# Optimization experiments

Measured on AMD Instinct MI355X. Metric: run time of the kernel, lower is better.

Reference implementation:

```python
import jax, jax.numpy as jnp
import numpy as np


def _igd(x, pf):
    # pf: [M, d] reference front, x: [N, d] candidate set
    # squared Euclidean distances via ||a||^2 + ||b||^2 - 2 a.b (cdist expansion)
    pf_sq = jnp.sum(pf * pf, axis=1, keepdims=True)          # [M, 1]
    x_sq = jnp.sum(x * x, axis=1, keepdims=True).T            # [1, N]
    cross = pf @ x.T                                          # [M, N]
    d2 = jnp.maximum(pf_sq + x_sq - 2.0 * cross, 0.0)
    dist = jnp.sqrt(d2)                                       # [M, N]
    # IGD: mean over reference points of min distance to candidate set
    return jnp.mean(jnp.min(dist, axis=1))


def setup_inputs() -> dict:
    key = jax.random.key(0)
    k1, k2 = jax.random.split(key)
    N, M, D = 16384, 16384, 64
    x = jax.random.normal(k1, (N, D), dtype=jnp.float32)
    pf = jax.random.normal(k2, (M, D), dtype=jnp.float32)
    return {"x": x, "pf": pf}


def reference(x, pf):
    return _igd(x, pf)
```

## Files before the change

kernel.cpp:

```cpp
#include <hip/hip_runtime.h>


typedef float f32x16 __attribute__((ext_vector_type(16)));
typedef int i32x8 __attribute__((ext_vector_type(8)));
typedef unsigned long long u64;

#define DIM 64
#define NSPLIT 12
#define UNITB 2048
#define CHUNKU 8
#define CHUNKB (CHUNKU * UNITB)
#define MTILE 256

union BFrag { u64 q[4]; i32x8 v; };

__device__ inline unsigned char enc_e4m3(float f) {
    unsigned int u = __float_as_uint(f);
    unsigned int s = (u >> 24) & 0x80u;
    unsigned int a = u & 0x7FFFFFFFu;
    if ((a >> 23) >= 121u) {
        unsigned int lsb = (a >> 20) & 1u;
        unsigned int r = a + 0x7FFFFu + lsb;
        int e = (int)(r >> 23) - 120;
        unsigned int m = (r >> 20) & 7u;
        if (e > 15 || (e == 15 && m == 7u)) return (unsigned char)(s | 0x7Eu);
        return (unsigned char)(s | ((unsigned)e << 3) | m);
    }
    int m = (int)rintf(__uint_as_float(a) * 512.0f);
    return (unsigned char)(s | (unsigned)m);
}

__device__ inline float dec_e4m3(unsigned char b) {
    int e = (b >> 3) & 15, m = b & 7;
    float v = e ? __uint_as_float((unsigned)((e + 120) << 23) | ((unsigned)m << 20))
                : (float)m * 0.001953125f;
    return (b & 0x80) ? -v : v;
}

__global__ void pack_kernel(const float* __restrict__ x, const float* __restrict__ pf,
                            unsigned char* __restrict__ Bp, unsigned char* __restrict__ Ab,
                            float* __restrict__ xsq, float* __restrict__ pfsq,
                            float* __restrict__ out, int N, int M) {
    int gid = blockIdx.x * blockDim.x + threadIdx.x;
    if (gid == 0) out[0] = 0.f;
    if (gid < N * 4) {
        int col = gid >> 2, t = gid & 3;
        const float* s = x + (size_t)col * DIM + t * 16;
        float partial = 0.f;
        u64 w[2] = {0, 0};
#pragma unroll
        for (int h = 0; h < 2; ++h) {
            float4 v0 = *(const float4*)(s + h * 8);
            float4 v1 = *(const float4*)(s + h * 8 + 4);
            float f[8] = {v0.x, v0.y, v0.z, v0.w, v1.x, v1.y, v1.z, v1.w};
#pragma unroll
            for (int j = 0; j < 8; ++j) {
                unsigned char b = enc_e4m3(f[j]);
                w[h] |= (u64)b << (8 * j);
                float d = dec_e4m3(b);
                partial += d * d;
            }
        }
        int u = col >> 5, c31 = col & 31;
        unsigned char* ub = Bp + (size_t)u * UNITB;
        int h = t >> 1;
#pragma unroll
        for (int ss = 0; ss < 2; ++ss) {
            int q = (t & 1) * 2 + ss;
            *(u64*)(ub + (size_t)q * 512 + (size_t)(h * 32 + c31) * 8) = w[ss];
        }
        partial += __shfl_xor(partial, 1);
        partial += __shfl_xor(partial, 2);
        if (t == 0) xsq[col] = partial;
    } else {
        int g = gid - N * 4;
        int row = g >> 2, q = g & 3;
        if (row >= M) return;
        const float* s = pf + (size_t)row * DIM + q * 16;
        float partial = 0.f;
        u64 w[2] = {0, 0};
#pragma unroll
        for (int h = 0; h < 2; ++h) {
            float4 v0 = *(const float4*)(s + h * 8);
            float4 v1 = *(const float4*)(s + h * 8 + 4);
            float f[8] = {v0.x, v0.y, v0.z, v0.w, v1.x, v1.y, v1.z, v1.w};
#pragma unroll
            for (int j = 0; j < 8; ++j) {
                unsigned char b = enc_e4m3(f[j] * -2.f);
                w[h] |= (u64)b << (8 * j);
                float d = dec_e4m3(b);
                partial += d * d;
            }
        }
        *(u64*)(Ab + (size_t)row * DIM + q * 16)     = w[0];
        *(u64*)(Ab + (size_t)row * DIM + q * 16 + 8) = w[1];
        partial += __shfl_xor(partial, 1);
        partial += __shfl_xor(partial, 2);
        if (q == 0) pfsq[row] = partial * 0.25f;
    }
}

__global__ __launch_bounds__(256, 3)
void igd_main(const unsigned char* __restrict__ A, const unsigned char* __restrict__ Bp,
              const float* __restrict__ xsq, float* __restrict__ partial, int N) {
    __shared__ unsigned char ldsB[2][CHUNKB];
    __shared__ float ldsX[2][CHUNKU * 32];
    const int tid = threadIdx.x;
    const int mTile  = blockIdx.x;
    const int nsplit = blockIdx.y;
    const int lane = tid & 63;
    const int wave = tid >> 6;
    const int half = lane >> 5;
    const int l31  = lane & 31;
    const int rowBase = mTile * MTILE + wave * 64;

    const int utotal = N / 32;
    const int ubase  = utotal / NSPLIT;
    const int urem   = utotal % NSPLIT;
    const int ustart = nsplit * ubase + (nsplit < urem ? nsplit : urem);
    const int ucount = ubase + (nsplit < urem ? 1 : 0);
    const int nch = (ucount + CHUNKU - 1) / CHUNKU;

    BFrag a[2];
#pragma unroll
    for (int g = 0; g < 2; ++g) {
        const unsigned char* ap = A + (size_t)(rowBase + 32 * g + l31) * DIM + half * 32;
#pragma unroll
        for (int qq = 0; qq < 4; ++qq)
            a[g].q[qq] = *(const u64*)(ap + qq * 8);
    }

    const unsigned char* gB = Bp + (size_t)ustart * UNITB;
    const float* gX = xsq + ustart * 32;

#define STAGE(c, buf)                                                          \
    {                                                                          \
        int bytes = (ucount - (c) * CHUNKU) < CHUNKU ? (ucount - (c) * CHUNKU) * UNITB : CHUNKB; \
        const unsigned char* src = gB + (size_t)(c) * CHUNKB;                  \
        _Pragma("unroll")                                                      \
        for (int i = 0; i < 4; ++i) {                                          \
            int off = i * 4096 + tid * 16;                                     \
            if (off < bytes)                                                   \
                *(float4*)(&ldsB[buf][off]) = *(const float4*)(src + off);     \
        }                                                                      \
        int xcnt = bytes >> 6;                                                 \
        if (tid < xcnt) ldsX[buf][tid] = gX[(c) * (CHUNKU * 32) + tid];        \
    }

    f32x16 zero, m0, m1;
#pragma unroll
    for (int r = 0; r < 16; ++r) { zero[r] = 0.f; m0[r] = 1e30f; m1[r] = 1e30f; }

#define LOADF(rr, lb, u)                                                       \
    {                                                                          \
        const unsigned char* p = (lb) + (u) * UNITB;                           \
        rr.q[0] = *(const u64*)(p);                                            \
        rr.q[1] = *(const u64*)(p + 512);                                      \
        rr.q[2] = *(const u64*)(p + 1024);                                     \
        rr.q[3] = *(const u64*)(p + 1536);                                     \
    }

#define MFMA2(accA, accB, bfrag)                                               \
    {                                                                          \
        accA = __builtin_amdgcn_mfma_scale_f32_32x32x64_f8f6f4(                \
            a[0].v, bfrag.v, zero, 0, 0, 0, 0x7F7F7F7F, 0, 0x7F7F7F7F);        \
        accB = __builtin_amdgcn_mfma_scale_f32_32x32x64_f8f6f4(                \
            a[1].v, bfrag.v, zero, 0, 0, 0, 0x7F7F7F7F, 0, 0x7F7F7F7F);        \
    }

#define MINS(accA, accB, xq)                                                   \
    {                                                                          \
        _Pragma("unroll")                                                      \
        for (int r = 0; r < 16; ++r) {                                         \
            m0[r] = fminf(m0[r], accA[r] + (xq));                              \
            m1[r] = fminf(m1[r], accB[r] + (xq));                              \
        }                                                                      \
    }

    STAGE(0, 0);
    __syncthreads();

    for (int c = 0; c < nch; ++c) {
        const int buf = c & 1;
        if (c + 1 < nch) STAGE(c + 1, buf ^ 1);
        const int cnt = (ucount - c * CHUNKU) < CHUNKU ? (ucount - c * CHUNKU) : CHUNKU;
        const unsigned char* lb = &ldsB[buf][0] + lane * 8;
        const float* lx = &ldsX[buf][0] + l31;
        if (cnt == CHUNKU) {
            BFrag bb0, bb1;
            f32x16 acA0, acA1, acB0, acB1;
            float xqA, xqB;
            LOADF(bb0, lb, 0); xqA = lx[0];
            LOADF(bb1, lb, 1); xqB = lx[32];
            MFMA2(acA0, acA1, bb0);
#pragma unroll
            for (int u = 0; u < CHUNKU; u += 2) {
                if (u + 2 < CHUNKU) LOADF(bb0, lb, u + 2);
                MFMA2(acB0, acB1, bb1);
                MINS(acA0, acA1, xqA);
                if (u + 2 < CHUNKU) xqA = lx[(u + 2) * 32];
                if (u + 3 < CHUNKU) LOADF(bb1, lb, u + 3);
                if (u + 2 < CHUNKU) MFMA2(acA0, acA1, bb0);
                MINS(acB0, acB1, xqB);
                if (u + 3 < CHUNKU) xqB = lx[(u + 3) * 32];
            }
        } else {
            BFrag bt;
            f32x16 t0, t1;
            for (int u = 0; u < cnt; ++u) {
                LOADF(bt, lb, u);
                MFMA2(t0, t1, bt);
                MINS(t0, t1, lx[u * 32]);
            }
        }
        __syncthreads();
    }
#undef STAGE
#undef LOADF
#undef MFMA2
#undef MINS

#pragma unroll
    for (int mask = 1; mask <= 16; mask <<= 1) {
#pragma unroll
        for (int r = 0; r < 16; ++r) {
            m0[r] = fminf(m0[r], __shfl_xor(m0[r], mask));
            m1[r] = fminf(m1[r], __shfl_xor(m1[r], mask));
        }
    }
    if (l31 == 0) {
#pragma unroll
        for (int r = 0; r < 16; ++r) {
            int row0 = rowBase + (r & 3) + 8 * (r >> 2) + 4 * half;
            partial[(size_t)row0 * NSPLIT + nsplit] = m0[r];
            partial[(size_t)(row0 + 32) * NSPLIT + nsplit] = m1[r];
        }
    }
}

__global__ void reduce_kernel(const float* __restrict__ partial, const float* __restrict__ pfsq,
                              float* __restrict__ out, int M, float invM) {
    int row = blockIdx.x * blockDim.x + threadIdx.x;
    float v = 0.f;
    if (row < M) {
        const float* p = partial + (size_t)row * NSPLIT;
        float mn = 3.4e38f;
#pragma unroll
        for (int s = 0; s < NSPLIT; ++s) mn = fminf(mn, p[s]);
        float d2 = mn + pfsq[row];
        v = sqrtf(fmaxf(d2, 0.f)) * invM;
    }
#pragma unroll
    for (int m = 1; m < 64; m <<= 1) v += __shfl_xor(v, m);
    __shared__ float wsum[4];
    int lane = threadIdx.x & 63, w = threadIdx.x >> 6;
    if (lane == 0) wsum[w] = v;
    __syncthreads();
    if (threadIdx.x == 0) atomicAdd(out, wsum[0] + wsum[1] + wsum[2] + wsum[3]);
}

extern "C" void kernel_launch(void* const* d_in, const int* in_sizes, int n_in,
                              void* d_out, int out_size, void* d_ws, size_t ws_size,
                              hipStream_t stream) {
    const float* x  = (const float*)d_in[0];
    const float* pf = (const float*)d_in[1];
    const int N = in_sizes[0] / DIM;
    const int M = in_sizes[1] / DIM;

    char* ws = (char*)d_ws;
    unsigned char* Bp = (unsigned char*)ws;
    unsigned char* Ab = (unsigned char*)(ws + (size_t)N * DIM);
    float* xsq  = (float*)(ws + (size_t)(N + M) * DIM);
    float* pfsq = xsq + N;
    float* part = pfsq + M;

    int packThreads = (N + M) * 4;
    pack_kernel<<<dim3((packThreads + 255) / 256), 256, 0, stream>>>(
        x, pf, Bp, Ab, xsq, pfsq, (float*)d_out, N, M);
    igd_main<<<dim3(M / MTILE, NSPLIT), 256, 0, stream>>>(Ab, Bp, xsq, part, N);
    reduce_kernel<<<dim3((M + 255) / 256), 256, 0, stream>>>(part, pfsq, (float*)d_out, M, 1.f / (float)M);
}
```

Measured before the change: 96.80 us.

## Stage B tiles via direct global-to-LDS loads and simplify MFMA software pipeline

```diff
diff --git a/kernel.cpp b/kernel.cpp
--- a/kernel.cpp
+++ b/kernel.cpp
@@ -13,6 +13,17 @@
 #define MTILE 256
 
 union BFrag { u64 q[4]; i32x8 v; };
+
+__device__ __forceinline__ void g2lds16(const void* g, void* l) {
+    __builtin_amdgcn_global_load_lds(
+        (const __attribute__((address_space(1))) unsigned int*)g,
+        (__attribute__((address_space(3))) unsigned int*)l, 16, 0, 0);
+}
+__device__ __forceinline__ void g2lds4(const void* g, void* l) {
+    __builtin_amdgcn_global_load_lds(
+        (const __attribute__((address_space(1))) unsigned int*)g,
+        (__attribute__((address_space(3))) unsigned int*)l, 4, 0, 0);
+}
 
 __device__ inline unsigned char enc_e4m3(float f) {
     unsigned int u = __float_as_uint(f);
@@ -141,10 +152,11 @@
         for (int i = 0; i < 4; ++i) {                                          \
             int off = i * 4096 + tid * 16;                                     \
             if (off < bytes)                                                   \
-                *(float4*)(&ldsB[buf][off]) = *(const float4*)(src + off);     \
+                g2lds16(src + off, &ldsB[buf][off]);                           \
         }                                                                      \
         int xcnt = bytes >> 6;                                                 \
-        if (tid < xcnt) ldsX[buf][tid] = gX[(c) * (CHUNKU * 32) + tid];        \
+        if (tid < xcnt)                                                        \
+            g2lds4(gX + (c) * (CHUNKU * 32) + tid, &ldsX[buf][tid]);           \
     }
 
     f32x16 zero, m0, m1;
@@ -187,28 +199,24 @@
         const unsigned char* lb = &ldsB[buf][0] + lane * 8;
         const float* lx = &ldsX[buf][0] + l31;
         if (cnt == CHUNKU) {
-            BFrag bb0, bb1;
-            f32x16 acA0, acA1, acB0, acB1;
-            float xqA, xqB;
-            LOADF(bb0, lb, 0); xqA = lx[0];
-            LOADF(bb1, lb, 1); xqB = lx[32];
-            MFMA2(acA0, acA1, bb0);
+            BFrag b0, b1;
+            LOADF(b0, lb, 0);
 #pragma unroll
             for (int u = 0; u < CHUNKU; u += 2) {
-                if (u + 2 < CHUNKU) LOADF(bb0, lb, u + 2);
-                MFMA2(acB0, acB1, bb1);
-                MINS(acA0, acA1, xqA);
-                if (u + 2 < CHUNKU) xqA = lx[(u + 2) * 32];
-                if (u + 3 < CHUNKU) LOADF(bb1, lb, u + 3);
-                if (u + 2 < CHUNKU) MFMA2(acA0, acA1, bb0);
-                MINS(acB0, acB1, xqB);
-                if (u + 3 < CHUNKU) xqB = lx[(u + 3) * 32];
+                LOADF(b1, lb, u + 1);
+                f32x16 acA0, acA1;
+                MFMA2(acA0, acA1, b0);
+                MINS(acA0, acA1, lx[u * 32]);
+                if (u + 2 < CHUNKU) LOADF(b0, lb, u + 2);
+                f32x16 acB0, acB1;
+                MFMA2(acB0, acB1, b1);
+                MINS(acB0, acB1, lx[(u + 1) * 32]);
             }
         } else {
             BFrag bt;
-            f32x16 t0, t1;
             for (int u = 0; u < cnt; ++u) {
                 LOADF(bt, lb, u);
+                f32x16 t0, t1;
                 MFMA2(t0, t1, bt);
                 MINS(t0, t1, lx[u * 32]);
             }
```

Result: faster. 90.25 us (-6.8%).
